# Optimization experiments

Measured on AMD Instinct MI355X. Metric: run time of the kernel, lower is better.

The kernel has to match this reference:

```python
import jax, jax.numpy as jnp
import numpy as np

NEG_INF = -jnp.inf

def log_g(x):
    # where(x>=0, log(relu(x)+0.5), -softplus(-x)); relu(x)+0.5 >= 0.5 so log is safe everywhere
    return jnp.where(x >= 0, jnp.log(jax.nn.relu(x) + 0.5), -jax.nn.softplus(-x))

def _combine(e1, e2):
    # resettable log-space affine combine: h <- exp(logA)*h + exp(logB), reset zeroes history
    a1, b1, r1 = e1
    a2, b2, r2 = e2
    a_in = jnp.where(r2, jnp.zeros_like(a1), a1)
    b_in = jnp.where(r2, jnp.full_like(b1, NEG_INF), b1)
    return (a2 + a_in, jnp.logaddexp(a2 + b_in, b2), r1 | r2)

def setup_inputs() -> dict:
    key = jax.random.key(0)
    k1, k2, k3, k4 = jax.random.split(key, 4)
    B, T, D_in, H, D_out = 8, 4096, 1024, 1024, 1024
    x = jax.random.normal(k1, (B, T, D_in), dtype=jnp.float32)
    is_init = jax.random.uniform(k2, (B, T)) < 0.005  # sparse episode resets
    W_hg = jax.random.normal(k3, (D_in, 2 * H), dtype=jnp.float32) / np.sqrt(D_in)
    W_out = jax.random.normal(k4, (H, D_out), dtype=jnp.float32) / np.sqrt(H)
    return {"x": x, "is_init": is_init, "W_hg": W_hg, "W_out": W_out}

def reference(x, is_init, W_hg, W_out):
    # training path: h_0 = 0 (log_h_0 = -inf), seq_len > 1
    hg = jnp.einsum('btd,dk->btk', x, W_hg)            # [B,T,2H]
    hidden, gate = jnp.split(hg, 2, axis=-1)           # each [B,T,H]
    log_coeffs = -jax.nn.softplus(gate)                # log(1 - z)
    log_values = -jax.nn.softplus(-gate) + log_g(hidden)  # log z + log g(h~)
    resets = jnp.broadcast_to(is_init[:, :, None], log_coeffs.shape)
    _, logB, _ = jax.lax.associative_scan(_combine, (log_coeffs, log_values, resets), axis=1)
    # h_t = logaddexp(logA_t + log_h0, logB_t); log_h0 = -inf since h_0 = 0 => h_t = exp(logB_t)
    h = jnp.exp(logB)                                  # [B,T,H]
    out = jnp.einsum('bth,ho->bto', h, W_out)          # [B,T,D_out]
    h_n = h[:, -1:]                                    # [B,1,H]
    return out, h_n
```

## Files before the change

### kernel.cpp

```cpp
#include <hip/hip_runtime.h>
#include <stdint.h>

#define B_    8
#define T_    4096
#define DIN   1024
#define HCH   1024
#define DOUT  1024
#define M_    (B_*T_)
#define CL    64
#define NCH   (T_/CL)

typedef unsigned short u16;
typedef unsigned int   u32;
typedef __attribute__((ext_vector_type(8))) __bf16 bf16x8;
typedef __attribute__((ext_vector_type(4))) float  f32x4;

static __device__ __forceinline__ u16 f2bf(float f){
  unsigned u = __builtin_bit_cast(unsigned, f);
  return (u16)((u + 0x7FFFu + ((u >> 16) & 1u)) >> 16);
}
static __device__ __forceinline__ float bf2f(u16 h){
  return __builtin_bit_cast(float, ((unsigned)h) << 16);
}

#define GLOAD_LDS16(gp, lp) __builtin_amdgcn_global_load_lds( \
    (__attribute__((address_space(1))) void*)(gp),            \
    (__attribute__((address_space(3))) void*)(lp), 16, 0, 0)

#define BARRIER() do { __builtin_amdgcn_sched_barrier(0); \
                       __builtin_amdgcn_s_barrier();      \
                       __builtin_amdgcn_sched_barrier(0); } while(0)

__global__ void cvt_bf16_kernel(const float* __restrict__ in, u16* __restrict__ out, int n4){
  int i = blockIdx.x * blockDim.x + threadIdx.x;
  if (i >= n4) return;
  float4 v = ((const float4*)in)[i];
  ushort4 o;
  o.x = f2bf(v.x); o.y = f2bf(v.y); o.z = f2bf(v.z); o.w = f2bf(v.w);
  ((ushort4*)out)[i] = o;
}

__global__ void transpose_cvt_kernel(const float* __restrict__ in, u16* __restrict__ out,
                                     int R, int C){
  __shared__ float tile[32][33];
  int tx = threadIdx.x & 31, ty = threadIdx.x >> 5;
  int c0 = blockIdx.x * 32, r0 = blockIdx.y * 32;
  #pragma unroll
  for (int j = 0; j < 4; ++j)
    tile[ty + j*8][tx] = in[(size_t)(r0 + ty + j*8) * C + c0 + tx];
  __syncthreads();
  #pragma unroll
  for (int j = 0; j < 4; ++j)
    out[(size_t)(c0 + ty + j*8) * R + r0 + tx] = f2bf(tile[tx][ty + j*8]);
}

__global__ void detect_kernel(const u32* __restrict__ p, int* __restrict__ flag){
  __shared__ int s;
  if (threadIdx.x == 0) s = 0;
  __syncthreads();
  int f = 0;
  for (int i = threadIdx.x; i < (B_*T_)/4; i += 1024)
    if (p[i] & 0xFFFFFF00u) f = 1;
  if (f) atomicOr(&s, 1);
  __syncthreads();
  if (threadIdx.x == 0) *flag = s;
}

template<bool BF16OUT, int NOUT>
__global__ __launch_bounds__(512, 2) void gemm8p_kernel(
    const u16* __restrict__ A, const u16* __restrict__ BT, void* __restrict__ outv)
{
  __shared__ u16 As[2][16384];
  __shared__ u16 Bs[2][16384];

  const int tid = threadIdx.x, lane = tid & 63, w = tid >> 6;
  const int wm = w >> 2, wn = w & 3;
  const int lr = lane & 15, lg = lane >> 4;
  const int l8 = lane >> 3, l7 = lane & 7;
  const int sgcol = (l7 ^ l8) * 8;

  const int nwg = gridDim.x;
  const int wg  = ((int)blockIdx.x & 7) * (nwg >> 3) + ((int)blockIdx.x >> 3);
  const int mb  = wg & 127;
  const int nb  = wg >> 7;
  const int m0  = mb * 256, n0 = nb * 256;

  const u16* __restrict__ Ab = A  + (size_t)m0 * 1024;
  const u16* __restrict__ Bb = BT + (size_t)n0 * 1024;

  auto stage = [&](u16 (*S)[16384], int buf, int half, int tt, const u16* __restrict__ Gb){
    #pragma unroll
    for (int i = 0; i < 2; ++i){
      int wi = w*2 + i;
      GLOAD_LDS16(Gb + (size_t)(half*128 + wi*8 + l8) * 1024 + tt*64 + sgcol,
                  &S[buf][half*8192 + wi*512]);
    }
  };

  bf16x8 af[4][2], b0[2][2], b1[2][2];
  f32x4 acc[2][2][4][2];
  #pragma unroll
  for (int a = 0; a < 2; ++a)
    #pragma unroll
    for (int b = 0; b < 2; ++b)
      #pragma unroll
      for (int m = 0; m < 4; ++m)
        #pragma unroll
        for (int n = 0; n < 2; ++n)
          acc[a][b][m][n] = (f32x4){0.f,0.f,0.f,0.f};

  auto ldA = [&](int buf, int mh){
    #pragma unroll
    for (int m = 0; m < 4; ++m)
      #pragma unroll
      for (int ks = 0; ks < 2; ++ks){
        int R = mh*128 + wm*64 + m*16 + lr;
        int g = (ks*4 + lg) ^ (lr & 7);
        af[m][ks] = *(const bf16x8*)&As[buf][R*64 + g*8];
      }
  };
  auto ldB = [&](bf16x8 (&bv)[2][2], int buf, int nh){
    #pragma unroll
    for (int n = 0; n < 2; ++n)
      #pragma unroll
      for (int ks = 0; ks < 2; ++ks){
        int R = nh*128 + wn*32 + n*16 + lr;
        int g = (ks*4 + lg) ^ (lr & 7);
        bv[n][ks] = *(const bf16x8*)&Bs[buf][R*64 + g*8];
      }
  };
  auto mmaQ = [&](f32x4 (&ac)[4][2], bf16x8 (&bv)[2][2]){
    __builtin_amdgcn_s_setprio(1);
    #pragma unroll
    for (int m = 0; m < 4; ++m)
      #pragma unroll
      for (int n = 0; n < 2; ++n)
        #pragma unroll
        for (int ks = 0; ks < 2; ++ks)
          ac[m][n] = __builtin_amdgcn_mfma_f32_16x16x32_bf16(af[m][ks], bv[n][ks], ac[m][n], 0, 0, 0);
    __builtin_amdgcn_s_setprio(0);
  };

  stage(As, 0, 0, 0, Ab);
  stage(Bs, 0, 0, 0, Bb);
  stage(Bs, 0, 1, 0, Bb);
  stage(As, 0, 1, 0, Ab);
  stage(As, 1, 0, 1, Ab);
  stage(Bs, 1, 0, 1, Bb);
  stage(Bs, 1, 1, 1, Bb);
  asm volatile("s_waitcnt vmcnt(6)" ::: "memory");
  BARRIER();

  for (int t = 0; t < 16; ++t){
    int cur = t & 1;
    ldA(cur, 0);
    ldB(b0, cur, 0);
    if (t+1 < 16) stage(As, cur^1, 1, t+1, Ab);
    BARRIER();
    mmaQ(acc[0][0], b0);
    BARRIER();
    ldB(b1, cur, 1);
    if (t+2 < 16) stage(As, cur, 0, t+2, Ab);
    BARRIER();
    mmaQ(acc[0][1], b1);
    BARRIER();
    ldA(cur, 1);
    if (t+2 < 16) stage(Bs, cur, 0, t+2, Bb);
    BARRIER();
    mmaQ(acc[1][1], b1);
    BARRIER();
    if (t+2 < 16) stage(Bs, cur, 1, t+2, Bb);
    if (t < 14)       { asm volatile("s_waitcnt vmcnt(6)" ::: "memory"); }
    else if (t == 14) { asm volatile("s_waitcnt vmcnt(0)" ::: "memory"); }
    BARRIER();
    mmaQ(acc[1][0], b0);
    BARRIER();
  }

  #pragma unroll
  for (int mh = 0; mh < 2; ++mh)
    #pragma unroll
    for (int nh = 0; nh < 2; ++nh)
      #pragma unroll
      for (int m = 0; m < 4; ++m)
        #pragma unroll
        for (int n = 0; n < 2; ++n)
          #pragma unroll
          for (int r = 0; r < 4; ++r){
            int row = m0 + mh*128 + wm*64 + m*16 + lg*4 + r;
            int col = n0 + nh*128 + wn*32 + n*16 + lr;
            float v = acc[mh][nh][m][n][r];
            if (BF16OUT) ((u16*)outv)[(size_t)row * NOUT + col] = f2bf(v);
            else       ((float*)outv)[(size_t)row * NOUT + col] = v;
          }
}

static __device__ __forceinline__ void cv_from_hg(float hv, float gv, float& c, float& v){
  c = 1.f / (1.f + __expf(gv));
  float z = 1.f - c;
  float g = (hv >= 0.f) ? (hv + 0.5f) : (1.f / (1.f + __expf(-hv)));
  v = z * g;
}

__global__ void scanA_kernel(const u16* __restrict__ hg,
                             const void* __restrict__ isin, const int* __restrict__ mode,
                             float* __restrict__ Cc, float* __restrict__ Vc)
{
  int tid = blockIdx.x * 256 + threadIdx.x;
  int chp = tid & 511, b = (tid >> 9) & 7, ck = tid >> 12;
  int ch0 = chp * 2;
  int md = *mode;
  const unsigned char* ib = (const unsigned char*)isin;
  const int* ii = (const int*)isin;
  int t0 = b * T_ + ck * CL;
  float C0 = 1.f, V0 = 0.f, C1 = 1.f, V1 = 0.f;
  #pragma unroll 4
  for (int i = 0; i < CL; ++i){
    int t = t0 + i;
    const u16* rowp = hg + (size_t)t * 2048;
    u32 h2 = *(const u32*)(rowp + ch0);
    u32 g2 = *(const u32*)(rowp + 1024 + ch0);
    float c0, v0, c1, v1;
    cv_from_hg(bf2f((u16)h2), bf2f((u16)(h2 >> 16)) * 0.f + bf2f((u16)(g2 & 0xFFFF)) * 0.f + bf2f((u16)h2), 0.f ? c0 : c0, v0);
    {
      float hv0 = bf2f((u16)(h2 & 0xFFFF)), hv1 = bf2f((u16)(h2 >> 16));
      float gv0 = bf2f((u16)(g2 & 0xFFFF)), gv1 = bf2f((u16)(g2 >> 16));
      cv_from_hg(hv0, gv0, c0, v0);
      cv_from_hg(hv1, gv1, c1, v1);
    }
    int r = md ? (int)ib[t] : ii[t];
    if (r){ C0 = 0.f; V0 = v0; C1 = 0.f; V1 = v1; }
    else  { V0 = __fmaf_rn(c0, V0, v0); C0 *= c0;
            V1 = __fmaf_rn(c1, V1, v1); C1 *= c1; }
  }
  int o = ck * 8192 + b * 1024 + ch0;
  *(float2*)&Cc[o] = make_float2(C0, C1);
  *(float2*)&Vc[o] = make_float2(V0, V1);
}

__global__ void scanB_kernel(const float* __restrict__ Cc, const float* __restrict__ Vc,
                             float* __restrict__ hin)
{
  int idx = blockIdx.x * 256 + threadIdx.x;
  float h = 0.f;
  #pragma unroll 8
  for (int ck = 0; ck < NCH; ++ck){
    int o = ck * 8192 + idx;
    hin[o] = h;
    h = __fmaf_rn(Cc[o], h, Vc[o]);
  }
}

__global__ void scanC_kernel(const u16* __restrict__ hg,
                             const void* __restrict__ isin, const int* __restrict__ mode,
                             const float* __restrict__ hin,
                             u16* __restrict__ hbf, float* __restrict__ hn)
{
  int tid = blockIdx.x * 256 + threadIdx.x;
  int chp = tid & 511, b = (tid >> 9) & 7, ck = tid >> 12;
  int ch0 = chp * 2;
  int md = *mode;
  const unsigned char* ib = (const unsigned char*)isin;
  const int* ii = (const int*)isin;
  int t0 = b * T_ + ck * CL;
  int o = ck * 8192 + b * 1024 + ch0;
  float h0 = hin[o], h1 = hin[o + 1];
  #pragma unroll 4
  for (int i = 0; i < CL; ++i){
    int t = t0 + i;
    const u16* rowp = hg + (size_t)t * 2048;
    u32 h2 = *(const u32*)(rowp + ch0);
    u32 g2 = *(const u32*)(rowp + 1024 + ch0);
    float hv0 = bf2f((u16)(h2 & 0xFFFF)), hv1 = bf2f((u16)(h2 >> 16));
    float gv0 = bf2f((u16)(g2 & 0xFFFF)), gv1 = bf2f((u16)(g2 >> 16));
    float c0, v0, c1, v1;
    cv_from_hg(hv0, gv0, c0, v0);
    cv_from_hg(hv1, gv1, c1, v1);
    int r = md ? (int)ib[t] : ii[t];
    h0 = r ? v0 : __fmaf_rn(c0, h0, v0);
    h1 = r ? v1 : __fmaf_rn(c1, h1, v1);
    *(u32*)&hbf[(size_t)t * HCH + ch0] = (u32)f2bf(h0) | ((u32)f2bf(h1) << 16);
  }
  if (ck == NCH - 1){ hn[b * 1024 + ch0] = h0; hn[b * 1024 + ch0 + 1] = h1; }
}

extern "C" void kernel_launch(void* const* d_in, const int* in_sizes, int n_in,
                              void* d_out, int out_size, void* d_ws, size_t ws_size,
                              hipStream_t stream)
{
  const float* x    = (const float*)d_in[0];
  const void*  isin = d_in[1];
  const float* Whg  = (const float*)d_in[2];
  const float* Wout = (const float*)d_in[3];
  float* out = (float*)d_out;

  char* ws = (char*)d_ws;
  size_t off = 0;
  auto alloc = [&](size_t bytes) -> char* {
    char* p = ws + off;
    off += (bytes + 255) & ~(size_t)255;
    return p;
  };
  u16*   xbf   = (u16*)  alloc((size_t)M_ * DIN * 2);
  u16*   WThg  = (u16*)  alloc((size_t)2 * HCH * DIN * 2);
  u16*   WTout = (u16*)  alloc((size_t)DOUT * HCH * 2);
  u16*   hg    = (u16*)  alloc((size_t)M_ * 2 * HCH * 2);
  u16*   hbf   = (u16*)  alloc((size_t)M_ * HCH * 2);
  float* Cc    = (float*)alloc((size_t)NCH * 8192 * 4);
  float* Vc    = (float*)alloc((size_t)NCH * 8192 * 4);
  float* hin   = (float*)alloc((size_t)NCH * 8192 * 4);
  int*   mode  = (int*)  alloc(256);
  (void)ws_size; (void)in_sizes; (void)n_in; (void)out_size;

  detect_kernel<<<1, 1024, 0, stream>>>((const u32*)isin, mode);
  cvt_bf16_kernel<<<(M_*DIN/4 + 255)/256, 256, 0, stream>>>(x, xbf, M_*DIN/4);
  transpose_cvt_kernel<<<dim3(2*HCH/32, DIN/32), 256, 0, stream>>>(Whg, WThg, DIN, 2*HCH);
  transpose_cvt_kernel<<<dim3(DOUT/32, HCH/32), 256, 0, stream>>>(Wout, WTout, HCH, DOUT);
  gemm8p_kernel<true, 2048><<<1024, 512, 0, stream>>>(xbf, WThg, hg);
  scanA_kernel<<<(8192*NCH/2)/256, 256, 0, stream>>>(hg, isin, mode, Cc, Vc);
  scanB_kernel<<<8192/256, 256, 0, stream>>>(Cc, Vc, hin);
  scanC_kernel<<<(8192*NCH/2)/256, 256, 0, stream>>>(hg, isin, mode, hin, hbf,
                                                     out + (size_t)M_ * DOUT);
  gemm8p_kernel<false, 1024><<<512, 512, 0, stream>>>(hbf, WTout, out);
}
```

Before: 604.8 us.

## Merge preprocessing kernels and vectorize GEMM epilogue stores via swapped MFMA operands

Four small preprocessing launches (flag detection, x conversion, two weight transposes) become one launch whose blocks pick a role from their block index. This removes launch gaps and lets the tiny work overlap. The GEMM swaps the MFMA A/B operands so each lane holds four consecutive columns, which lets the epilogue emit one 8- or 16-byte vector store instead of four scalar stores. It also drops a dead duplicate cv_from_hg call in scanA. The merged launch puts one long-running serial detect block alongside thousands of short blocks.

```diff
diff --git a/kernel.cpp b/kernel.cpp
--- a/kernel.cpp
+++ b/kernel.cpp
@@ -31,20 +31,12 @@
                        __builtin_amdgcn_s_barrier();      \
                        __builtin_amdgcn_sched_barrier(0); } while(0)
 
-__global__ void cvt_bf16_kernel(const float* __restrict__ in, u16* __restrict__ out, int n4){
-  int i = blockIdx.x * blockDim.x + threadIdx.x;
-  if (i >= n4) return;
-  float4 v = ((const float4*)in)[i];
-  ushort4 o;
-  o.x = f2bf(v.x); o.y = f2bf(v.y); o.z = f2bf(v.z); o.w = f2bf(v.w);
-  ((ushort4*)out)[i] = o;
-}
-
-__global__ void transpose_cvt_kernel(const float* __restrict__ in, u16* __restrict__ out,
-                                     int R, int C){
+static __device__ __forceinline__ void transpose_tile(const float* __restrict__ in,
+                                                      u16* __restrict__ out,
+                                                      int R, int C, int bx, int by){
   __shared__ float tile[32][33];
   int tx = threadIdx.x & 31, ty = threadIdx.x >> 5;
-  int c0 = blockIdx.x * 32, r0 = blockIdx.y * 32;
+  int c0 = bx * 32, r0 = by * 32;
   #pragma unroll
   for (int j = 0; j < 4; ++j)
     tile[ty + j*8][tx] = in[(size_t)(r0 + ty + j*8) * C + c0 + tx];
@@ -54,16 +46,38 @@
     out[(size_t)(c0 + ty + j*8) * R + r0 + tx] = f2bf(tile[tx][ty + j*8]);
 }
 
-__global__ void detect_kernel(const u32* __restrict__ p, int* __restrict__ flag){
-  __shared__ int s;
-  if (threadIdx.x == 0) s = 0;
-  __syncthreads();
-  int f = 0;
-  for (int i = threadIdx.x; i < (B_*T_)/4; i += 1024)
-    if (p[i] & 0xFFFFFF00u) f = 1;
-  if (f) atomicOr(&s, 1);
-  __syncthreads();
-  if (threadIdx.x == 0) *flag = s;
+__global__ void prep_kernel(const float* __restrict__ x, u16* __restrict__ xbf,
+                            const float* __restrict__ Whg, const float* __restrict__ Wout,
+                            const u32* __restrict__ isin,
+                            u16* __restrict__ WThg, u16* __restrict__ WTout,
+                            int* __restrict__ flag){
+  int bid = blockIdx.x;
+  if (bid < 2048){
+    transpose_tile(Whg, WThg, DIN, 2*HCH, bid & 63, bid >> 6);
+  } else if (bid < 3072){
+    int b2 = bid - 2048;
+    transpose_tile(Wout, WTout, HCH, DOUT, b2 & 31, b2 >> 5);
+  } else if (bid == 3072){
+    __shared__ int s;
+    if (threadIdx.x == 0) s = 0;
+    __syncthreads();
+    int f = 0;
+    for (int i = threadIdx.x; i < (B_*T_)/4; i += 256)
+      if (isin[i] & 0xFFFFFF00u) f = 1;
+    if (f) atomicOr(&s, 1);
+    __syncthreads();
+    if (threadIdx.x == 0) *flag = s;
+  } else {
+    int cb = bid - 3073;
+    #pragma unroll
+    for (int k = 0; k < 4; ++k){
+      int i = (cb*4 + k)*256 + threadIdx.x;
+      float4 v = ((const float4*)x)[i];
+      ushort4 o;
+      o.x = f2bf(v.x); o.y = f2bf(v.y); o.z = f2bf(v.z); o.w = f2bf(v.w);
+      ((ushort4*)xbf)[i] = o;
+    }
+  }
 }
 
 template<bool BF16OUT, int NOUT>
@@ -81,8 +95,7 @@
 
   const int nwg = gridDim.x;
   const int wg  = ((int)blockIdx.x & 7) * (nwg >> 3) + ((int)blockIdx.x >> 3);
-  const int mb  = wg & 127;
-  const int nb  = wg >> 7;
+  const int mb  = wg & 127, nb = wg >> 7;
   const int m0  = mb * 256, n0 = nb * 256;
 
   const u16* __restrict__ Ab = A  + (size_t)m0 * 1024;
@@ -137,7 +150,7 @@
       for (int n = 0; n < 2; ++n)
         #pragma unroll
         for (int ks = 0; ks < 2; ++ks)
-          ac[m][n] = __builtin_amdgcn_mfma_f32_16x16x32_bf16(af[m][ks], bv[n][ks], ac[m][n], 0, 0, 0);
+          ac[m][n] = __builtin_amdgcn_mfma_f32_16x16x32_bf16(bv[n][ks], af[m][ks], ac[m][n], 0, 0, 0);
     __builtin_amdgcn_s_setprio(0);
   };
 
@@ -180,19 +193,24 @@
   #pragma unroll
   for (int mh = 0; mh < 2; ++mh)
     #pragma unroll
-    for (int nh = 0; nh < 2; ++nh)
-      #pragma unroll
-      for (int m = 0; m < 4; ++m)
+    for (int m = 0; m < 4; ++m){
+      int row = m0 + mh*128 + wm*64 + m*16 + lr;
+      #pragma unroll
+      for (int nh = 0; nh < 2; ++nh)
         #pragma unroll
-        for (int n = 0; n < 2; ++n)
-          #pragma unroll
-          for (int r = 0; r < 4; ++r){
-            int row = m0 + mh*128 + wm*64 + m*16 + lg*4 + r;
-            int col = n0 + nh*128 + wn*32 + n*16 + lr;
-            float v = acc[mh][nh][m][n][r];
-            if (BF16OUT) ((u16*)outv)[(size_t)row * NOUT + col] = f2bf(v);
-            else       ((float*)outv)[(size_t)row * NOUT + col] = v;
+        for (int n = 0; n < 2; ++n){
+          int col = n0 + nh*128 + wn*32 + n*16 + lg*4;
+          f32x4 v = acc[mh][nh][m][n];
+          if (BF16OUT){
+            ushort4 p;
+            p.x = f2bf(v[0]); p.y = f2bf(v[1]); p.z = f2bf(v[2]); p.w = f2bf(v[3]);
+            *(ushort4*)&((u16*)outv)[(size_t)row * NOUT + col] = p;
+          } else {
+            float4 p = make_float4(v[0], v[1], v[2], v[3]);
+            *(float4*)&((float*)outv)[(size_t)row * NOUT + col] = p;
           }
+        }
+    }
 }
 
 static __device__ __forceinline__ void cv_from_hg(float hv, float gv, float& c, float& v){
@@ -220,14 +238,11 @@
     const u16* rowp = hg + (size_t)t * 2048;
     u32 h2 = *(const u32*)(rowp + ch0);
     u32 g2 = *(const u32*)(rowp + 1024 + ch0);
+    float hv0 = bf2f((u16)(h2 & 0xFFFF)), hv1 = bf2f((u16)(h2 >> 16));
+    float gv0 = bf2f((u16)(g2 & 0xFFFF)), gv1 = bf2f((u16)(g2 >> 16));
     float c0, v0, c1, v1;
-    cv_from_hg(bf2f((u16)h2), bf2f((u16)(h2 >> 16)) * 0.f + bf2f((u16)(g2 & 0xFFFF)) * 0.f + bf2f((u16)h2), 0.f ? c0 : c0, v0);
-    {
-      float hv0 = bf2f((u16)(h2 & 0xFFFF)), hv1 = bf2f((u16)(h2 >> 16));
-      float gv0 = bf2f((u16)(g2 & 0xFFFF)), gv1 = bf2f((u16)(g2 >> 16));
-      cv_from_hg(hv0, gv0, c0, v0);
-      cv_from_hg(hv1, gv1, c1, v1);
-    }
+    cv_from_hg(hv0, gv0, c0, v0);
+    cv_from_hg(hv1, gv1, c1, v1);
     int r = md ? (int)ib[t] : ii[t];
     if (r){ C0 = 0.f; V0 = v0; C1 = 0.f; V1 = v1; }
     else  { V0 = __fmaf_rn(c0, V0, v0); C0 *= c0;
@@ -312,10 +327,8 @@
   int*   mode  = (int*)  alloc(256);
   (void)ws_size; (void)in_sizes; (void)n_in; (void)out_size;
 
-  detect_kernel<<<1, 1024, 0, stream>>>((const u32*)isin, mode);
-  cvt_bf16_kernel<<<(M_*DIN/4 + 255)/256, 256, 0, stream>>>(x, xbf, M_*DIN/4);
-  transpose_cvt_kernel<<<dim3(2*HCH/32, DIN/32), 256, 0, stream>>>(Whg, WThg, DIN, 2*HCH);
-  transpose_cvt_kernel<<<dim3(DOUT/32, HCH/32), 256, 0, stream>>>(Wout, WTout, HCH, DOUT);
+  prep_kernel<<<11265, 256, 0, stream>>>(x, xbf, Whg, Wout, (const u32*)isin,
+                                         WThg, WTout, mode);
   gemm8p_kernel<true, 2048><<<1024, 512, 0, stream>>>(xbf, WThg, hg);
   scanA_kernel<<<(8192*NCH/2)/256, 256, 0, stream>>>(hg, isin, mode, Cc, Vc);
   scanB_kernel<<<8192/256, 256, 0, stream>>>(Cc, Vc, hin);
```

After: 613.2 us. About the same (+1.4%).
